# Kernel tuning notes

Hardware: AMD Instinct MI355X
Metric: run time of the kernel (lower is better)

Reference implementation:

```python
import jax, jax.numpy as jnp
import numpy as np

B, X, Y, Z, C = 1, 16, 16, 16, 768
NUM_HEADS = 12


def setup_inputs() -> dict:
    key = jax.random.key(0)
    k0, k1, k2 = jax.random.split(key, 3)
    x = jax.random.normal(k0, (B, X, Y, Z, C), dtype=jnp.float32)
    # Linear weights stored as [in, out] (torch stores [out, in]; math is x @ W_in_out + b)
    w_qkv = jax.random.normal(k1, (C, 3 * C), dtype=jnp.float32) * 0.02
    b_qkv = jnp.zeros((3 * C,), dtype=jnp.float32)
    w_proj = jax.random.normal(k2, (C, C), dtype=jnp.float32) * 0.02
    b_proj = jnp.zeros((C,), dtype=jnp.float32)
    return {"x": x, "w_qkv": w_qkv, "b_qkv": b_qkv, "w_proj": w_proj, "b_proj": b_proj}


def reference(x, w_qkv, b_qkv, w_proj, b_proj):
    b, xx, yy, zz, c = x.shape
    h = NUM_HEADS
    hd = c // h
    scale = hd ** (-0.5)
    n = xx * yy * zz  # flatten 3D grid into tokens

    qkv = x.reshape(b, n, c) @ w_qkv + b_qkv          # [B, N, 3C]
    qkv = qkv.reshape(b, n, 3, h, hd).transpose(2, 0, 3, 1, 4)  # [3, B, H, N, hd]
    q, k, v = qkv[0], qkv[1], qkv[2]

    attn = jnp.einsum('bhnd,bhmd->bhnm', q * scale, k)  # [B, H, N, N]
    attn = jax.nn.softmax(attn, axis=-1)
    out = jnp.einsum('bhnm,bhmd->bhnd', attn, v)        # [B, H, N, hd]
    out = out.transpose(0, 2, 1, 3).reshape(b, n, c)
    out = out @ w_proj + b_proj
    return out.reshape(b, xx, yy, zz, c)
```

## Files before the change

kernel.cpp:

```cpp
#include <hip/hip_runtime.h>
#include <cstddef>

#define N_TOK 4096
#define C_DIM 768
#define H_NUM 12
#define C3    2304

typedef unsigned short u16;
using short8  = __attribute__((ext_vector_type(8))) short;
using floatx4 = __attribute__((ext_vector_type(4))) float;
using u16x4   = __attribute__((ext_vector_type(4))) u16;
using uint2v  = __attribute__((ext_vector_type(2))) unsigned;

#define K2SCALE 0.18033688011112043f

__device__ __forceinline__ u16 f2bf(float f) {
  union { float f; unsigned u; } v; v.f = f;
  unsigned r = v.u + 0x7FFFu + ((v.u >> 16) & 1u);
  return (u16)(r >> 16);
}

__device__ __forceinline__ unsigned permpack(float a, float b) {
  union { float f; unsigned u; } x, y; x.f = a; y.f = b;
  return __builtin_amdgcn_perm(y.u, x.u, 0x07060302u);
}

__device__ __forceinline__ float aexp2(float x) {
  float r;
  asm("v_exp_f32 %0, %1" : "=v"(r) : "v"(x));
  return r;
}

__device__ __forceinline__ float arcp(float x) {
  float r;
  asm("v_rcp_f32 %0, %1" : "=v"(r) : "v"(x));
  return r;
}

__device__ __forceinline__ void gload_lds16(const void* g, void* l) {
  __builtin_amdgcn_global_load_lds(
      (const __attribute__((address_space(1))) unsigned int*)g,
      (__attribute__((address_space(3))) unsigned int*)l, 16, 0, 0);
}

__global__ void k_pre(const float* __restrict__ x, u16* __restrict__ xb,
                      const float* __restrict__ wq, u16* __restrict__ wqT,
                      const float* __restrict__ wp, u16* __restrict__ wpT) {
  __shared__ float tile[32][33];
  const int b = blockIdx.x;
  if (b < 3072) {
    int i = b * 256 + threadIdx.x;
    float4 f = ((const float4*)x)[i];
    u16x4 o;
    o[0] = f2bf(f.x); o[1] = f2bf(f.y); o[2] = f2bf(f.z); o[3] = f2bf(f.w);
    ((u16x4*)xb)[i] = o;
    return;
  }
  const float* in; u16* out; int Cc, bx, by;
  if (b < 4800) { int t = b - 3072; in = wq; out = wqT; Cc = 2304; bx = t % 72; by = t / 72; }
  else          { int t = b - 4800; in = wp; out = wpT; Cc = 768;  bx = t % 24; by = t / 24; }
  const int R = 768;
  const int tx = threadIdx.x & 31;
  const int ty = threadIdx.x >> 5;
  const int c0 = bx * 32, r0 = by * 32;
#pragma unroll
  for (int i = 0; i < 32; i += 8)
    tile[ty + i][tx] = in[(size_t)(r0 + ty + i) * Cc + c0 + tx];
  __syncthreads();
#pragma unroll
  for (int i = 0; i < 32; i += 8)
    out[(size_t)(c0 + ty + i) * R + r0 + tx] = f2bf(tile[tx][ty + i]);
}

template <int MODE>
__global__ __launch_bounds__(256)
void k_gemm_bt(const u16* __restrict__ A, const u16* __restrict__ B,
               const float* __restrict__ bias, void* __restrict__ outp,
               u16* __restrict__ vT, int K) {
  __shared__ u16 As[128 * 32];
  __shared__ u16 Bs[128 * 32];
  const int tid  = threadIdx.x;
  const int wave = tid >> 6, lane = tid & 63, quad = lane >> 4, l16 = lane & 15;
  const int wrow = wave >> 1, wcol = wave & 1;
  const int bm = blockIdx.y, bn = blockIdx.x;
  const int r3 = l16 & 3;

  floatx4 acc[4][4];
#pragma unroll
  for (int i = 0; i < 4; ++i)
#pragma unroll
    for (int j = 0; j < 4; ++j)
#pragma unroll
      for (int r = 0; r < 4; ++r) acc[i][j][r] = 0.f;

  const int ar = tid >> 2;
  const int ac = ((tid & 3) ^ (ar & 3)) * 8;
  const u16* gA = A + (size_t)(bm * 128 + ar) * K + ac;
  const u16* gB = B + (size_t)(bn * 128 + ar) * K + ac;
  u16* lA = &As[0] + tid * 8;
  u16* lB = &Bs[0] + tid * 8;

  for (int k0 = 0; k0 < K; k0 += 32) {
    gload_lds16(gA + k0,                  lA);
    gload_lds16(gA + k0 + (size_t)64 * K, lA + 2048);
    gload_lds16(gB + k0,                  lB);
    gload_lds16(gB + k0 + (size_t)64 * K, lB + 2048);
    __syncthreads();
    short8 af[4], bf[4];
#pragma unroll
    for (int t = 0; t < 4; ++t) {
      af[t] = *(const short8*)&As[(wrow * 64 + t * 16 + l16) * 32 + ((quad ^ r3) * 8)];
      bf[t] = *(const short8*)&Bs[(wcol * 64 + t * 16 + l16) * 32 + ((quad ^ r3) * 8)];
    }
#pragma unroll
    for (int tm = 0; tm < 4; ++tm)
#pragma unroll
      for (int tn = 0; tn < 4; ++tn)
        acc[tm][tn] = __builtin_amdgcn_mfma_f32_16x16x32_bf16(af[tm], bf[tn], acc[tm][tn], 0, 0, 0);
    __syncthreads();
  }

  if (MODE == 0) {
    u16* qkv = (u16*)outp;
    const float qs = (bn < 6) ? K2SCALE : 1.0f;
#pragma unroll
    for (int tn = 0; tn < 4; ++tn) {
      const int col = bn * 128 + wcol * 64 + tn * 16 + l16;
      const float bc = bias[col];
      if (col < 1536) {
#pragma unroll
        for (int tm = 0; tm < 4; ++tm) {
          const int rowb = bm * 128 + wrow * 64 + tm * 16 + quad * 4;
#pragma unroll
          for (int r = 0; r < 4; ++r)
            qkv[(size_t)(rowb + r) * C3 + col] = f2bf((acc[tm][tn][r] + bc) * qs);
        }
      } else {
        const int hd_ = col - 1536;
#pragma unroll
        for (int tm = 0; tm < 4; ++tm) {
          const int rowb = bm * 128 + wrow * 64 + tm * 16 + quad * 4;
          u16x4 pk;
#pragma unroll
          for (int r = 0; r < 4; ++r) pk[r] = f2bf(acc[tm][tn][r] + bc);
          *(u16x4*)&vT[(size_t)hd_ * N_TOK + rowb] = pk;
        }
      }
    }
  } else {
    float* out = (float*)outp;
#pragma unroll
    for (int tn = 0; tn < 4; ++tn) {
      const int col = bn * 128 + wcol * 64 + tn * 16 + l16;
      const float bc = bias[col];
#pragma unroll
      for (int tm = 0; tm < 4; ++tm) {
        const int rowb = bm * 128 + wrow * 64 + tm * 16 + quad * 4;
#pragma unroll
        for (int r = 0; r < 4; ++r)
          out[(size_t)(rowb + r) * C_DIM + col] = acc[tm][tn][r] + bc;
      }
    }
  }
}

__global__ __launch_bounds__(256)
void k_flash(const u16* __restrict__ qkv, const u16* __restrict__ vT,
             float* __restrict__ Opart, float* __restrict__ lpart) {
  __shared__ u16 Ks[2][64 * 64];
  __shared__ u16 Vs[2][64 * 64];
  __shared__ u16 Ps[4][32 * 64];
  const int tid  = threadIdx.x;
  const int wave = tid >> 6, lane = tid & 63, quad = lane >> 4, l16 = lane & 15;
  const int qt = blockIdx.x, h = blockIdx.y, split = blockIdx.z;
  const int lr = tid >> 3;
  const int lc = ((tid & 7) ^ (lr & 7)) * 8;
  const int r7 = l16 & 7;
  const int kb = split * 2048;

  short8 bq[2][2];
#pragma unroll
  for (int qs = 0; qs < 2; ++qs)
#pragma unroll
    for (int ks = 0; ks < 2; ++ks)
      bq[qs][ks] = *(const short8*)&qkv[(size_t)(qt * 128 + wave * 32 + qs * 16 + l16) * C3
                                        + h * 64 + ks * 32 + quad * 8];

  const u16* gk = qkv + (size_t)lr * C3 + C_DIM + h * 64 + lc;
  const u16* gv = vT + (size_t)(h * 64 + lr) * N_TOK + lc;

  auto stage = [&](int b, int m0) {
#pragma unroll
    for (int p = 0; p < 2; ++p) {
      gload_lds16(gk + (size_t)(m0 + p * 32) * C3,    &Ks[b][p * 2048 + tid * 8]);
      gload_lds16(gv + (size_t)(p * 32) * N_TOK + m0, &Vs[b][p * 2048 + tid * 8]);
    }
  };

  floatx4 o0[4], o1[4], l0, l1, zv;
#pragma unroll
  for (int r = 0; r < 4; ++r) { zv[r] = 0.f; l0[r] = 0.f; l1[r] = 0.f; }
#pragma unroll
  for (int d = 0; d < 4; ++d)
#pragma unroll
    for (int r = 0; r < 4; ++r) { o0[d][r] = 0.f; o1[d][r] = 0.f; }

  short8 ones;
#pragma unroll
  for (int i = 0; i < 8; ++i) ones[i] = (short)0x3F80;

  u16* psw = &Ps[wave][0];

  auto compute = [&](int b) __attribute__((always_inline)) {
    const u16* kbp = &Ks[b][0];
    const u16* vb  = &Vs[b][0];
    floatx4 s0[4], s1[4];
#pragma unroll
    for (int tn = 0; tn < 4; ++tn) {
      short8 ak = *(const short8*)&kbp[(tn * 16 + l16) * 64 + (quad ^ r7) * 8];
      s0[tn] = __builtin_amdgcn_mfma_f32_16x16x32_bf16(ak, bq[0][0], zv, 0, 0, 0);
      s1[tn] = __builtin_amdgcn_mfma_f32_16x16x32_bf16(ak, bq[1][0], zv, 0, 0, 0);
    }
#pragma unroll
    for (int tn = 0; tn < 4; ++tn) {
      short8 ak = *(const short8*)&kbp[(tn * 16 + l16) * 64 + ((quad + 4) ^ r7) * 8];
      s0[tn] = __builtin_amdgcn_mfma_f32_16x16x32_bf16(ak, bq[0][1], s0[tn], 0, 0, 0);
      s1[tn] = __builtin_amdgcn_mfma_f32_16x16x32_bf16(ak, bq[1][1], s1[tn], 0, 0, 0);
    }
#pragma unroll
    for (int qs = 0; qs < 2; ++qs) {
      u16* pr = psw + qs * 1024;
#pragma unroll
      for (int tn = 0; tn < 4; ++tn) {
        floatx4 sv = qs ? s1[tn] : s0[tn];
        float p0 = aexp2(sv[0]);
        float p1 = aexp2(sv[1]);
        float p2 = aexp2(sv[2]);
        float p3 = aexp2(sv[3]);
        uint2v pk;
        pk[0] = permpack(p0, p1);
        pk[1] = permpack(p2, p3);
        *(uint2v*)&pr[l16 * 64 + ((2 * tn + (quad >> 1)) ^ r7) * 8 + (quad & 1) * 4] = pk;
      }
    }
#pragma unroll
    for (int ks = 0; ks < 2; ++ks) {
      short8 ap0 = *(const short8*)&psw[l16 * 64 + ((quad + 4 * ks) ^ r7) * 8];
      short8 ap1 = *(const short8*)&psw[(16 + l16) * 64 + ((quad + 4 * ks) ^ r7) * 8];
#pragma unroll
      for (int dt = 0; dt < 4; ++dt) {
        short8 bv = *(const short8*)&vb[(dt * 16 + l16) * 64 + ((quad + 4 * ks) ^ r7) * 8];
        o0[dt] = __builtin_amdgcn_mfma_f32_16x16x32_bf16(ap0, bv, o0[dt], 0, 0, 0);
        o1[dt] = __builtin_amdgcn_mfma_f32_16x16x32_bf16(ap1, bv, o1[dt], 0, 0, 0);
      }
      l0 = __builtin_amdgcn_mfma_f32_16x16x32_bf16(ap0, ones, l0, 0, 0, 0);
      l1 = __builtin_amdgcn_mfma_f32_16x16x32_bf16(ap1, ones, l1, 0, 0, 0);
    }
  };

  stage(0, kb);
  __syncthreads();
  int m0 = kb + 64;
  for (int it2 = 0; it2 < 15; ++it2) {
    stage(1, m0); m0 += 64;
    compute(0);
    __syncthreads();
    stage(0, m0); m0 += 64;
    compute(1);
    __syncthreads();
  }
  stage(1, m0);
  compute(0);
  __syncthreads();
  compute(1);

  const int rowg = qt * 128 + wave * 32 + quad * 4;
  float* Ob = Opart + ((size_t)(split * H_NUM + h) * N_TOK) * 64;
  float* lb = lpart + (size_t)(split * H_NUM + h) * N_TOK;
#pragma unroll
  for (int r = 0; r < 4; ++r) {
#pragma unroll
    for (int dt = 0; dt < 4; ++dt) {
      const int col = dt * 16 + l16;
      Ob[(size_t)(rowg + r) * 64 + col]      = o0[dt][r];
      Ob[(size_t)(rowg + 16 + r) * 64 + col] = o1[dt][r];
    }
    if (l16 == 0) {
      lb[rowg + r]      = l0[r];
      lb[rowg + 16 + r] = l1[r];
    }
  }
}

__global__ void k_combine(const float* __restrict__ Op, const float* __restrict__ lp,
                          u16* __restrict__ ao) {
  const int idx = blockIdx.x * 256 + threadIdx.x;
  const int col = idx & 63;
  const int row = idx >> 6;
  const float o = Op[(size_t)row * 64 + col] + Op[((size_t)row + 49152) * 64 + col];
  const float l = lp[row] + lp[row + 49152];
  const int h = row >> 12, q = row & 4095;
  ao[(size_t)q * C_DIM + h * 64 + col] = f2bf(o * arcp(l));
}

extern "C" void kernel_launch(void* const* d_in, const int* in_sizes, int n_in,
                              void* d_out, int out_size, void* d_ws, size_t ws_size,
                              hipStream_t stream) {
  const float* x      = (const float*)d_in[0];
  const float* w_qkv  = (const float*)d_in[1];
  const float* b_qkv  = (const float*)d_in[2];
  const float* w_proj = (const float*)d_in[3];
  const float* b_proj = (const float*)d_in[4];
  float* out = (float*)d_out;

  u16* xb     = (u16*)d_ws;
  u16* wqkvT  = xb     + (size_t)N_TOK * C_DIM;
  u16* wprojT = wqkvT  + (size_t)C3 * C_DIM;
  u16* qkv    = wprojT + (size_t)C_DIM * C_DIM;
  u16* vT     = qkv    + (size_t)N_TOK * C3;
  u16* ao     = vT     + (size_t)C_DIM * N_TOK;
  float* Opart = (float*)(ao + (size_t)N_TOK * C_DIM);
  float* lpart = Opart + (size_t)2 * H_NUM * N_TOK * 64;

  k_pre<<<5376, 256, 0, stream>>>(x, xb, w_qkv, wqkvT, w_proj, wprojT);
  k_gemm_bt<0><<<dim3(C3 / 128, N_TOK / 128), 256, 0, stream>>>(xb, wqkvT, b_qkv, qkv, vT, C_DIM);
  k_flash<<<dim3(N_TOK / 128, H_NUM, 2), 256, 0, stream>>>(qkv, vT, Opart, lpart);
  k_combine<<<H_NUM * N_TOK * 64 / 256, 256, 0, stream>>>(Opart, lpart, ao);
  k_gemm_bt<1><<<dim3(C_DIM / 128, N_TOK / 128), 256, 0, stream>>>(ao, wprojT, b_proj, out, nullptr, C_DIM);
}
```

Before: 218.4 us.

## Widen flash attention query tile to 64 rows per wave and split keys four ways

Each wave now handles 64 query rows instead of 32, so every K/V tile staged into LDS is reused across twice as many queries. The key range is split into four parts instead of two, which keeps the grid at 768 blocks, and the combine kernel sums four partials. The P tile is processed in 32-key halves to limit LDS and register use. The costs are higher register pressure from 16 output accumulators per wave and doubled partial-output traffic into the combine step.

```diff
diff --git a/kernel.cpp b/kernel.cpp
--- a/kernel.cpp
+++ b/kernel.cpp
@@ -5,6 +5,7 @@
 #define C_DIM 768
 #define H_NUM 12
 #define C3    2304
+#define NSPL  4
 
 typedef unsigned short u16;
 using short8  = __attribute__((ext_vector_type(8))) short;
@@ -169,22 +170,24 @@
              float* __restrict__ Opart, float* __restrict__ lpart) {
   __shared__ u16 Ks[2][64 * 64];
   __shared__ u16 Vs[2][64 * 64];
-  __shared__ u16 Ps[4][32 * 64];
+  __shared__ u16 Ps[4][64 * 32];
   const int tid  = threadIdx.x;
   const int wave = tid >> 6, lane = tid & 63, quad = lane >> 4, l16 = lane & 15;
   const int qt = blockIdx.x, h = blockIdx.y, split = blockIdx.z;
   const int lr = tid >> 3;
   const int lc = ((tid & 7) ^ (lr & 7)) * 8;
   const int r7 = l16 & 7;
-  const int kb = split * 2048;
-
-  short8 bq[2][2];
-#pragma unroll
-  for (int qs = 0; qs < 2; ++qs)
-#pragma unroll
-    for (int ks = 0; ks < 2; ++ks)
-      bq[qs][ks] = *(const short8*)&qkv[(size_t)(qt * 128 + wave * 32 + qs * 16 + l16) * C3
-                                        + h * 64 + ks * 32 + quad * 8];
+  const int r3 = l16 & 3;
+  const int kb = split * (N_TOK / NSPL);
+  const int nt = (N_TOK / NSPL) / 64;
+
+  short8 bq[4][2];
+#pragma unroll
+  for (int qs = 0; qs < 4; ++qs)
+#pragma unroll
+    for (int dh = 0; dh < 2; ++dh)
+      bq[qs][dh] = *(const short8*)&qkv[(size_t)(qt * 256 + wave * 64 + qs * 16 + l16) * C3
+                                        + h * 64 + dh * 32 + quad * 8];
 
   const u16* gk = qkv + (size_t)lr * C3 + C_DIM + h * 64 + lc;
   const u16* gv = vT + (size_t)(h * 64 + lr) * N_TOK + lc;
@@ -197,13 +200,18 @@
     }
   };
 
-  floatx4 o0[4], o1[4], l0, l1, zv;
-#pragma unroll
-  for (int r = 0; r < 4; ++r) { zv[r] = 0.f; l0[r] = 0.f; l1[r] = 0.f; }
-#pragma unroll
-  for (int d = 0; d < 4; ++d)
-#pragma unroll
-    for (int r = 0; r < 4; ++r) { o0[d][r] = 0.f; o1[d][r] = 0.f; }
+  floatx4 o[4][4], l[4], zv;
+#pragma unroll
+  for (int r = 0; r < 4; ++r) zv[r] = 0.f;
+#pragma unroll
+  for (int qs = 0; qs < 4; ++qs) {
+#pragma unroll
+    for (int r = 0; r < 4; ++r) l[qs][r] = 0.f;
+#pragma unroll
+    for (int dt = 0; dt < 4; ++dt)
+#pragma unroll
+      for (int r = 0; r < 4; ++r) o[qs][dt][r] = 0.f;
+  }
 
   short8 ones;
 #pragma unroll
@@ -214,80 +222,70 @@
   auto compute = [&](int b) __attribute__((always_inline)) {
     const u16* kbp = &Ks[b][0];
     const u16* vb  = &Vs[b][0];
-    floatx4 s0[4], s1[4];
-#pragma unroll
-    for (int tn = 0; tn < 4; ++tn) {
-      short8 ak = *(const short8*)&kbp[(tn * 16 + l16) * 64 + (quad ^ r7) * 8];
-      s0[tn] = __builtin_amdgcn_mfma_f32_16x16x32_bf16(ak, bq[0][0], zv, 0, 0, 0);
-      s1[tn] = __builtin_amdgcn_mfma_f32_16x16x32_bf16(ak, bq[1][0], zv, 0, 0, 0);
-    }
-#pragma unroll
-    for (int tn = 0; tn < 4; ++tn) {
-      short8 ak = *(const short8*)&kbp[(tn * 16 + l16) * 64 + ((quad + 4) ^ r7) * 8];
-      s0[tn] = __builtin_amdgcn_mfma_f32_16x16x32_bf16(ak, bq[0][1], s0[tn], 0, 0, 0);
-      s1[tn] = __builtin_amdgcn_mfma_f32_16x16x32_bf16(ak, bq[1][1], s1[tn], 0, 0, 0);
-    }
-#pragma unroll
-    for (int qs = 0; qs < 2; ++qs) {
-      u16* pr = psw + qs * 1024;
-#pragma unroll
-      for (int tn = 0; tn < 4; ++tn) {
-        floatx4 sv = qs ? s1[tn] : s0[tn];
-        float p0 = aexp2(sv[0]);
-        float p1 = aexp2(sv[1]);
-        float p2 = aexp2(sv[2]);
-        float p3 = aexp2(sv[3]);
-        uint2v pk;
-        pk[0] = permpack(p0, p1);
-        pk[1] = permpack(p2, p3);
-        *(uint2v*)&pr[l16 * 64 + ((2 * tn + (quad >> 1)) ^ r7) * 8 + (quad & 1) * 4] = pk;
+#pragma unroll
+    for (int kh = 0; kh < 2; ++kh) {
+      short8 ak[2][2];
+#pragma unroll
+      for (int tl = 0; tl < 2; ++tl)
+#pragma unroll
+        for (int dh = 0; dh < 2; ++dh)
+          ak[tl][dh] = *(const short8*)&kbp[((kh * 2 + tl) * 16 + l16) * 64
+                                            + ((dh * 4 + quad) ^ r7) * 8];
+#pragma unroll
+      for (int qs = 0; qs < 4; ++qs) {
+        floatx4 s0 = __builtin_amdgcn_mfma_f32_16x16x32_bf16(ak[0][0], bq[qs][0], zv, 0, 0, 0);
+        floatx4 s1 = __builtin_amdgcn_mfma_f32_16x16x32_bf16(ak[1][0], bq[qs][0], zv, 0, 0, 0);
+        s0 = __builtin_amdgcn_mfma_f32_16x16x32_bf16(ak[0][1], bq[qs][1], s0, 0, 0, 0);
+        s1 = __builtin_amdgcn_mfma_f32_16x16x32_bf16(ak[1][1], bq[qs][1], s1, 0, 0, 0);
+        const int row = qs * 16 + l16;
+        unsigned pa0 = permpack(aexp2(s0[0]), aexp2(s0[1]));
+        unsigned pa1 = permpack(aexp2(s0[2]), aexp2(s0[3]));
+        unsigned pb0 = permpack(aexp2(s1[0]), aexp2(s1[1]));
+        unsigned pb1 = permpack(aexp2(s1[2]), aexp2(s1[3]));
+        uint2v w0; w0[0] = pa0; w0[1] = pa1;
+        uint2v w1; w1[0] = pb0; w1[1] = pb1;
+        *(uint2v*)&psw[row * 32 + (((quad >> 1)) ^ r3) * 8 + (quad & 1) * 4]     = w0;
+        *(uint2v*)&psw[row * 32 + ((2 + (quad >> 1)) ^ r3) * 8 + (quad & 1) * 4] = w1;
       }
-    }
-#pragma unroll
-    for (int ks = 0; ks < 2; ++ks) {
-      short8 ap0 = *(const short8*)&psw[l16 * 64 + ((quad + 4 * ks) ^ r7) * 8];
-      short8 ap1 = *(const short8*)&psw[(16 + l16) * 64 + ((quad + 4 * ks) ^ r7) * 8];
+      short8 ap[4];
+#pragma unroll
+      for (int qs = 0; qs < 4; ++qs)
+        ap[qs] = *(const short8*)&psw[(qs * 16 + l16) * 32 + ((quad ^ r3) * 8)];
 #pragma unroll
       for (int dt = 0; dt < 4; ++dt) {
-        short8 bv = *(const short8*)&vb[(dt * 16 + l16) * 64 + ((quad + 4 * ks) ^ r7) * 8];
-        o0[dt] = __builtin_amdgcn_mfma_f32_16x16x32_bf16(ap0, bv, o0[dt], 0, 0, 0);
-        o1[dt] = __builtin_amdgcn_mfma_f32_16x16x32_bf16(ap1, bv, o1[dt], 0, 0, 0);
+        short8 bv = *(const short8*)&vb[(dt * 16 + l16) * 64 + ((kh * 4 + quad) ^ r7) * 8];
+#pragma unroll
+        for (int qs = 0; qs < 4; ++qs)
+          o[qs][dt] = __builtin_amdgcn_mfma_f32_16x16x32_bf16(ap[qs], bv, o[qs][dt], 0, 0, 0);
       }
-      l0 = __builtin_amdgcn_mfma_f32_16x16x32_bf16(ap0, ones, l0, 0, 0, 0);
-      l1 = __builtin_amdgcn_mfma_f32_16x16x32_bf16(ap1, ones, l1, 0, 0, 0);
+#pragma unroll
+      for (int qs = 0; qs < 4; ++qs)
+        l[qs] = __builtin_amdgcn_mfma_f32_16x16x32_bf16(ap[qs], ones, l[qs], 0, 0, 0);
     }
   };
 
   stage(0, kb);
   __syncthreads();
   int m0 = kb + 64;
-  for (int it2 = 0; it2 < 15; ++it2) {
-    stage(1, m0); m0 += 64;
-    compute(0);
+  for (int t = 1; t < nt; ++t) {
+    stage(t & 1, m0);
+    m0 += 64;
+    compute((t - 1) & 1);
     __syncthreads();
-    stage(0, m0); m0 += 64;
-    compute(1);
-    __syncthreads();
-  }
-  stage(1, m0);
-  compute(0);
-  __syncthreads();
-  compute(1);
-
-  const int rowg = qt * 128 + wave * 32 + quad * 4;
+  }
+  compute((nt - 1) & 1);
+
   float* Ob = Opart + ((size_t)(split * H_NUM + h) * N_TOK) * 64;
   float* lb = lpart + (size_t)(split * H_NUM + h) * N_TOK;
 #pragma unroll
-  for (int r = 0; r < 4; ++r) {
-#pragma unroll
-    for (int dt = 0; dt < 4; ++dt) {
-      const int col = dt * 16 + l16;
-      Ob[(size_t)(rowg + r) * 64 + col]      = o0[dt][r];
-      Ob[(size_t)(rowg + 16 + r) * 64 + col] = o1[dt][r];
-    }
-    if (l16 == 0) {
-      lb[rowg + r]      = l0[r];
-      lb[rowg + 16 + r] = l1[r];
+  for (int qs = 0; qs < 4; ++qs) {
+    const int rowg = qt * 256 + wave * 64 + qs * 16 + quad * 4;
+#pragma unroll
+    for (int r = 0; r < 4; ++r) {
+#pragma unroll
+      for (int dt = 0; dt < 4; ++dt)
+        Ob[(size_t)(rowg + r) * 64 + dt * 16 + l16] = o[qs][dt][r];
+      if (l16 == 0) lb[rowg + r] = l[qs][r];
     }
   }
 }
@@ -297,8 +295,12 @@
   const int idx = blockIdx.x * 256 + threadIdx.x;
   const int col = idx & 63;
   const int row = idx >> 6;
-  const float o = Op[(size_t)row * 64 + col] + Op[((size_t)row + 49152) * 64 + col];
-  const float l = lp[row] + lp[row + 49152];
+  float o = 0.f, l = 0.f;
+#pragma unroll
+  for (int s = 0; s < NSPL; ++s) {
+    o += Op[((size_t)row + (size_t)s * H_NUM * N_TOK) * 64 + col];
+    l += lp[row + s * H_NUM * N_TOK];
+  }
   const int h = row >> 12, q = row & 4095;
   ao[(size_t)q * C_DIM + h * 64 + col] = f2bf(o * arcp(l));
 }
@@ -320,11 +322,11 @@
   u16* vT     = qkv    + (size_t)N_TOK * C3;
   u16* ao     = vT     + (size_t)C_DIM * N_TOK;
   float* Opart = (float*)(ao + (size_t)N_TOK * C_DIM);
-  float* lpart = Opart + (size_t)2 * H_NUM * N_TOK * 64;
+  float* lpart = Opart + (size_t)NSPL * H_NUM * N_TOK * 64;
 
   k_pre<<<5376, 256, 0, stream>>>(x, xb, w_qkv, wqkvT, w_proj, wprojT);
   k_gemm_bt<0><<<dim3(C3 / 128, N_TOK / 128), 256, 0, stream>>>(xb, wqkvT, b_qkv, qkv, vT, C_DIM);
-  k_flash<<<dim3(N_TOK / 128, H_NUM, 2), 256, 0, stream>>>(qkv, vT, Opart, lpart);
+  k_flash<<<dim3(N_TOK / 256, H_NUM, NSPL), 256, 0, stream>>>(qkv, vT, Opart, lpart);
   k_combine<<<H_NUM * N_TOK * 64 / 256, 256, 0, stream>>>(Opart, lpart, ao);
   k_gemm_bt<1><<<dim3(C_DIM / 128, N_TOK / 128), 256, 0, stream>>>(ao, wprojT, b_proj, out, nullptr, C_DIM);
 }
```

New measurement: 218.7 us. About the same (+0.1%).
